# Performance work log

Hardware: AMD Instinct MI355X
Metric: run time of the kernel (lower is better)

Reference implementation:

```python
import jax, jax.numpy as jnp
import numpy as np
from jax import lax

B, T = 64, 512
VOCAB, EMBED, UNITS = 32000, 256, 512


def setup_inputs() -> dict:
    key = jax.random.key(0)
    ks = jax.random.split(key, 8)
    s = 0.05
    G = 4 * UNITS
    return {
        "encoder_input": jax.random.randint(ks[0], (B, T), 0, VOCAB, dtype=jnp.int32),
        "embedding": jax.random.normal(ks[1], (VOCAB, EMBED), jnp.float32) * s,
        "W_fwd": jax.random.normal(ks[2], (EMBED, G), jnp.float32) * s,
        "U_fwd": jax.random.normal(ks[3], (UNITS, G), jnp.float32) * s,
        "b_fwd": jnp.zeros((G,), jnp.float32),
        "W_bwd": jax.random.normal(ks[4], (EMBED, G), jnp.float32) * s,
        "U_bwd": jax.random.normal(ks[5], (UNITS, G), jnp.float32) * s,
        "b_bwd": jnp.zeros((G,), jnp.float32),
    }


def _lstm_scan(x, mask, W, Uw, b, reverse):
    """Masked LSTM over time. Keras semantics: at masked steps the (h, c)
    state is carried through unchanged and the emitted output repeats the
    previous hidden state (which for LSTM equals the carried h).
    x: [B, T, E] float, mask: [B, T] bool."""
    Bsz = x.shape[0]
    Uh = Uw.shape[0]
    # Precompute input projection for all timesteps: [B, T, 4U]
    xz = jnp.einsum("bte,eg->btg", x, W) + b

    def step(carry, inp):
        h, c = carry
        z_x, m = inp  # z_x: [B, 4U], m: [B]
        z = z_x + h @ Uw
        i, f, g, o = jnp.split(z, 4, axis=-1)  # Keras gate order i, f, c, o
        i = jax.nn.sigmoid(i)
        f = jax.nn.sigmoid(f)
        g = jnp.tanh(g)
        o = jax.nn.sigmoid(o)
        c_new = f * c + i * g
        h_new = o * jnp.tanh(c_new)
        m = m[:, None]
        h = jnp.where(m, h_new, h)
        c = jnp.where(m, c_new, c)
        return (h, c), h

    h0 = jnp.zeros((Bsz, Uh), x.dtype)
    c0 = jnp.zeros((Bsz, Uh), x.dtype)
    (h, c), ys = lax.scan(
        step, (h0, c0), (xz.swapaxes(0, 1), mask.T), reverse=reverse
    )
    # lax.scan with reverse=True stacks outputs in original time order,
    # matching Keras Bidirectional's reverse-then-re-reverse behavior.
    return ys.swapaxes(0, 1), h, c


def reference(encoder_input, embedding, W_fwd, U_fwd, b_fwd, W_bwd, U_bwd, b_bwd):
    mask = encoder_input != 0  # mask_zero=True
    emb = embedding[encoder_input]  # [B, T, E]
    out_f, h_f, c_f = _lstm_scan(emb, mask, W_fwd, U_fwd, b_fwd, reverse=False)
    out_b, h_b, c_b = _lstm_scan(emb, mask, W_bwd, U_bwd, b_bwd, reverse=True)
    encoder_output = jnp.concatenate([out_f, out_b], axis=-1)  # [B, T, 2U]
    final_state_h = jnp.concatenate([h_f, h_b], axis=-1)  # [B, 2U]
    final_state_c = jnp.concatenate([c_f, c_b], axis=-1)  # [B, 2U]
    # Dropout is identity at inference (training=False default).
    return encoder_output, final_state_h, final_state_c
```

## Files before the change

kernel.cpp:

```cpp
#include <hip/hip_runtime.h>
#include <cstdint>


#define B_ 64
#define T_ 512
#define E_ 256

typedef __attribute__((ext_vector_type(8))) short bf16x8;
typedef __attribute__((ext_vector_type(4))) float f32x4;
typedef __attribute__((ext_vector_type(2))) float f32x2;
typedef __attribute__((ext_vector_type(2))) unsigned u32x2;

__device__ __forceinline__ unsigned short f2bf(float x) {
  unsigned u = __float_as_uint(x);
  u += 0x7FFFu + ((u >> 16) & 1u);
  return (unsigned short)(u >> 16);
}
__device__ __forceinline__ float sigm(float x) { return 1.0f / (1.0f + __expf(-x)); }
__device__ __forceinline__ float tanh_(float x) { return 1.0f - 2.0f / (__expf(2.0f * x) + 1.0f); }

__global__ void prep_kernel(const int* __restrict__ enc, const float* __restrict__ emb,
                            unsigned short* __restrict__ o) {
  const int bi = blockIdx.x;
  const int t = bi >> 6, b = bi & 63;
  const int tok = enc[b * T_ + t];
  float4 v = ((const float4*)(emb + (size_t)tok * E_))[threadIdx.x];
  ushort4 w;
  w.x = f2bf(v.x); w.y = f2bf(v.y); w.z = f2bf(v.z); w.w = f2bf(v.w);
  ((ushort4*)(o + (size_t)t * (B_ * E_) + b * E_))[threadIdx.x] = w;
}

__global__ void prep_w(const float* __restrict__ Wf, const float* __restrict__ Uf,
                       const float* __restrict__ Wb, const float* __restrict__ Ub,
                       unsigned short* __restrict__ Uq, unsigned short* __restrict__ Wq) {
  int bi = blockIdx.x;
  const int ns = bi & 1; bi >>= 1;
  const int kk = bi % 24; bi /= 24;
  const int nh = bi & 1; bi >>= 1;
  const int cg = bi & 31; bi >>= 5;
  const int d = bi;
  const int lane = threadIdx.x;
  const int l15 = lane & 15, l4 = lane >> 4;
  const bool isU = (kk < 16);
  const float* src = isU ? (d ? Ub : Uf) : (d ? Wb : Wf);
  const int ks = isU ? kk : (kk - 16);
  const int col = (nh * 2 + ns) * 512 + cg * 16 + l15;
  const int row0 = ks * 32 + l4 * 8;
  bf16x8 f;
#pragma unroll
  for (int i = 0; i < 8; ++i) f[i] = (short)f2bf(src[(size_t)(row0 + i) * 2048 + col]);
  unsigned short* dst = isU
    ? Uq + ((size_t)(((d * 32 + cg) * 2 + nh) * 16 + ks) * 2 + ns) * 512 + lane * 8
    : Wq + ((size_t)(((d * 32 + cg) * 2 + nh) * 8 + ks) * 2 + ns) * 512 + lane * 8;
  *(bf16x8*)dst = f;
}

__global__ __launch_bounds__(256, 1)
void lstm_dag(const int* __restrict__ enc, const unsigned short* __restrict__ embq,
              const unsigned short* __restrict__ Uq, const unsigned short* __restrict__ Wq,
              const float* __restrict__ bfv, const float* __restrict__ bbv,
              unsigned short* __restrict__ Hst, f32x2* __restrict__ SC,
              int* __restrict__ flg, float* __restrict__ out) {
  const int s = blockIdx.x >> 6;
  const int inner = blockIdx.x & 63;
  const int d = inner >> 5;
  const int cg = inner & 31;
  const int tid = threadIdx.x;
  const int lane = tid & 63;
  const int wave = tid >> 6;
  const int mh = wave & 1, nh = wave >> 1;
  const int l15 = lane & 15, l4 = lane >> 4;
  const int u0 = cg * 16;
  const int t = d ? (T_ - 1 - s) : s;

  __shared__ float Z[64][68];

  const unsigned short* ub = Uq + ((size_t)((d * 32 + cg) * 2 + nh)) * (16 * 2 * 512);
  const unsigned short* wb = Wq + ((size_t)((d * 32 + cg) * 2 + nh)) * (8 * 2 * 512);
  bf16x8 u_frag[16][2];
#pragma unroll
  for (int ks = 0; ks < 16; ++ks)
#pragma unroll
    for (int ns = 0; ns < 2; ++ns)
      u_frag[ks][ns] = *(const bf16x8*)(ub + (size_t)(ks * 2 + ns) * 512 + lane * 8);
  bf16x8 w_frag[8][2];
#pragma unroll
  for (int ks = 0; ks < 8; ++ks)
#pragma unroll
    for (int ns = 0; ns < 2; ++ns)
      w_frag[ks][ns] = *(const bf16x8*)(wb + (size_t)(ks * 2 + ns) * 512 + lane * 8);

  bf16x8 apf[8][2];
  {
    const unsigned short* eT = embq + (size_t)t * (B_ * E_);
#pragma unroll
    for (int ks = 0; ks < 8; ++ks)
#pragma unroll
      for (int ms = 0; ms < 2; ++ms) {
        const int b = mh * 32 + ms * 16 + l15;
        apf[ks][ms] = *(const bf16x8*)(eT + b * E_ + ks * 32 + l4 * 8);
      }
  }
  const int eb = tid >> 2;
  const int uq = tid & 3;
  const int msk = enc[eb * T_ + t];
  const float* bd = d ? bbv : bfv;
  f32x4 bias[4];
#pragma unroll
  for (int g = 0; g < 4; ++g)
    bias[g] = *(const f32x4*)(bd + g * 512 + u0 + uq * 4);

  f32x4 acc[2][2];
#pragma unroll
  for (int ms = 0; ms < 2; ++ms)
#pragma unroll
    for (int ns = 0; ns < 2; ++ns) acc[ms][ns] = (f32x4)0.0f;

#pragma unroll
  for (int ks = 0; ks < 8; ++ks)
#pragma unroll
    for (int ms = 0; ms < 2; ++ms)
#pragma unroll
      for (int ns = 0; ns < 2; ++ns)
        acc[ms][ns] = __builtin_amdgcn_mfma_f32_16x16x32_bf16(apf[ks][ms], w_frag[ks][ns],
                                                              acc[ms][ns], 0, 0, 0);

  f32x4 hin0 = (f32x4)0.0f, hin1 = (f32x4)0.0f;

  if (s > 0) {
    if (wave == 0) {
      int* fp = flg + ((size_t)s * 2 + d) * 32;
      for (;;) {
        int v = __hip_atomic_load(fp + (lane & 31), __ATOMIC_RELAXED, __HIP_MEMORY_SCOPE_AGENT);
        if (__ballot(v == 0) == 0ull) break;
        __builtin_amdgcn_s_sleep(4);
      }
    }
    __syncthreads();
    __builtin_amdgcn_s_setprio(1);

    bf16x8 ha[16][2];
    {
      const char* Hrd = (const char*)(Hst + ((size_t)(s & 1) * 2 + d) * 32768);
      const char* lb = Hrd + (l4 >> 1) * 2048 + mh * 1024 + l15 * 32 + (l4 & 1) * 16;
      const char* b0p = lb + 0 * 8192 + 4096;
      const char* b1p = lb + 1 * 8192 + 4096;
      const char* b2p = lb + 2 * 8192 + 4096;
      const char* b3p = lb + 3 * 8192 + 4096;
      const char* b4p = lb + 4 * 8192 + 4096;
      const char* b5p = lb + 5 * 8192 + 4096;
      const char* b6p = lb + 6 * 8192 + 4096;
      const char* b7p = lb + 7 * 8192 + 4096;
      const char* sp0 = (const char*)(SC + ((size_t)(s & 1) * 2 + d) * 32768
                                      + (size_t)cg * 1024 + eb * 16 + uq * 4);
      asm volatile(
        "global_load_dwordx4 %0, %34, off offset:-4096 sc0 sc1\n\t"
        "global_load_dwordx4 %1, %34, off offset:-3584 sc0 sc1\n\t"
        "global_load_dwordx4 %2, %34, off offset:0 sc0 sc1\n\t"
        "global_load_dwordx4 %3, %34, off offset:512 sc0 sc1\n\t"
        "global_load_dwordx4 %4, %35, off offset:-4096 sc0 sc1\n\t"
        "global_load_dwordx4 %5, %35, off offset:-3584 sc0 sc1\n\t"
        "global_load_dwordx4 %6, %35, off offset:0 sc0 sc1\n\t"
        "global_load_dwordx4 %7, %35, off offset:512 sc0 sc1\n\t"
        "global_load_dwordx4 %8, %36, off offset:-4096 sc0 sc1\n\t"
        "global_load_dwordx4 %9, %36, off offset:-3584 sc0 sc1\n\t"
        "global_load_dwordx4 %10, %36, off offset:0 sc0 sc1\n\t"
        "global_load_dwordx4 %11, %36, off offset:512 sc0 sc1\n\t"
        "global_load_dwordx4 %12, %37, off offset:-4096 sc0 sc1\n\t"
        "global_load_dwordx4 %13, %37, off offset:-3584 sc0 sc1\n\t"
        "global_load_dwordx4 %14, %37, off offset:0 sc0 sc1\n\t"
        "global_load_dwordx4 %15, %37, off offset:512 sc0 sc1\n\t"
        "global_load_dwordx4 %16, %38, off offset:-4096 sc0 sc1\n\t"
        "global_load_dwordx4 %17, %38, off offset:-3584 sc0 sc1\n\t"
        "global_load_dwordx4 %18, %38, off offset:0 sc0 sc1\n\t"
        "global_load_dwordx4 %19, %38, off offset:512 sc0 sc1\n\t"
        "global_load_dwordx4 %20, %39, off offset:-4096 sc0 sc1\n\t"
        "global_load_dwordx4 %21, %39, off offset:-3584 sc0 sc1\n\t"
        "global_load_dwordx4 %22, %39, off offset:0 sc0 sc1\n\t"
        "global_load_dwordx4 %23, %39, off offset:512 sc0 sc1\n\t"
        "global_load_dwordx4 %24, %40, off offset:-4096 sc0 sc1\n\t"
        "global_load_dwordx4 %25, %40, off offset:-3584 sc0 sc1\n\t"
        "global_load_dwordx4 %26, %40, off offset:0 sc0 sc1\n\t"
        "global_load_dwordx4 %27, %40, off offset:512 sc0 sc1\n\t"
        "global_load_dwordx4 %28, %41, off offset:-4096 sc0 sc1\n\t"
        "global_load_dwordx4 %29, %41, off offset:-3584 sc0 sc1\n\t"
        "global_load_dwordx4 %30, %41, off offset:0 sc0 sc1\n\t"
        "global_load_dwordx4 %31, %41, off offset:512 sc0 sc1\n\t"
        "global_load_dwordx4 %32, %42, off sc0 sc1\n\t"
        "global_load_dwordx4 %33, %42, off offset:16 sc0 sc1\n\t"
        "s_waitcnt vmcnt(0)"
        : "=v"(ha[0][0]), "=v"(ha[0][1]), "=v"(ha[1][0]), "=v"(ha[1][1]),
          "=v"(ha[2][0]), "=v"(ha[2][1]), "=v"(ha[3][0]), "=v"(ha[3][1]),
          "=v"(ha[4][0]), "=v"(ha[4][1]), "=v"(ha[5][0]), "=v"(ha[5][1]),
          "=v"(ha[6][0]), "=v"(ha[6][1]), "=v"(ha[7][0]), "=v"(ha[7][1]),
          "=v"(ha[8][0]), "=v"(ha[8][1]), "=v"(ha[9][0]), "=v"(ha[9][1]),
          "=v"(ha[10][0]), "=v"(ha[10][1]), "=v"(ha[11][0]), "=v"(ha[11][1]),
          "=v"(ha[12][0]), "=v"(ha[12][1]), "=v"(ha[13][0]), "=v"(ha[13][1]),
          "=v"(ha[14][0]), "=v"(ha[14][1]), "=v"(ha[15][0]), "=v"(ha[15][1]),
          "=v"(hin0), "=v"(hin1)
        : "v"(b0p), "v"(b1p), "v"(b2p), "v"(b3p),
          "v"(b4p), "v"(b5p), "v"(b6p), "v"(b7p), "v"(sp0)
        : "memory");
    }
#pragma unroll
    for (int ks = 0; ks < 16; ++ks) {
      acc[0][0] = __builtin_amdgcn_mfma_f32_16x16x32_bf16(ha[ks][0], u_frag[ks][0], acc[0][0], 0, 0, 0);
      acc[0][1] = __builtin_amdgcn_mfma_f32_16x16x32_bf16(ha[ks][0], u_frag[ks][1], acc[0][1], 0, 0, 0);
      acc[1][0] = __builtin_amdgcn_mfma_f32_16x16x32_bf16(ha[ks][1], u_frag[ks][0], acc[1][0], 0, 0, 0);
      acc[1][1] = __builtin_amdgcn_mfma_f32_16x16x32_bf16(ha[ks][1], u_frag[ks][1], acc[1][1], 0, 0, 0);
    }
  }

#pragma unroll
  for (int ms = 0; ms < 2; ++ms)
#pragma unroll
    for (int ns = 0; ns < 2; ++ns)
#pragma unroll
      for (int r = 0; r < 4; ++r)
        Z[mh * 32 + ms * 16 + l4 * 4 + r][nh * 32 + ns * 16 + l15] = acc[ms][ns][r];
  __syncthreads();

  f32x4 vi = *(const f32x4*)&Z[eb][uq * 4];
  f32x4 vf = *(const f32x4*)&Z[eb][16 + uq * 4];
  f32x4 vg = *(const f32x4*)&Z[eb][32 + uq * 4];
  f32x4 vo = *(const f32x4*)&Z[eb][48 + uq * 4];
  float hv[4], cv[4];
  {
    const bool m = (msk != 0);
    float hi_[4] = {hin0[0], hin0[2], hin1[0], hin1[2]};
    float ci_[4] = {hin0[1], hin0[3], hin1[1], hin1[3]};
#pragma unroll
    for (int i = 0; i < 4; ++i) {
      float ig = sigm(vi[i] + bias[0][i]);
      float fg = sigm(vf[i] + bias[1][i]);
      float gg = tanh_(vg[i] + bias[2][i]);
      float og = sigm(vo[i] + bias[3][i]);
      float cn = fg * ci_[i] + ig * gg;
      float hn = og * tanh_(cn);
      hv[i] = m ? hn : hi_[i];
      cv[i] = m ? cn : ci_[i];
    }
  }

  {
    u32x2 hu;
    hu[0] = (unsigned)f2bf(hv[0]) | ((unsigned)f2bf(hv[1]) << 16);
    hu[1] = (unsigned)f2bf(hv[2]) | ((unsigned)f2bf(hv[3]) << 16);
    f32x4 sc0v, sc1v;
    sc0v[0] = hv[0]; sc0v[1] = cv[0]; sc0v[2] = hv[1]; sc0v[3] = cv[1];
    sc1v[0] = hv[2]; sc1v[1] = cv[2]; sc1v[2] = hv[3]; sc1v[3] = cv[3];
    char* hp = (char*)(Hst + ((size_t)((s + 1) & 1) * 2 + d) * 32768
                       + (size_t)cg * 1024 + eb * 16 + uq * 4);
    char* scp = (char*)(SC + ((size_t)((s + 1) & 1) * 2 + d) * 32768
                        + (size_t)cg * 1024 + eb * 16 + uq * 4);
    asm volatile(
      "global_store_dwordx2 %0, %2, off sc0 sc1\n\t"
      "global_store_dwordx4 %1, %3, off sc0 sc1\n\t"
      "global_store_dwordx4 %1, %4, off offset:16 sc0 sc1\n\t"
      "s_waitcnt vmcnt(0)"
      :: "v"(hp), "v"(scp), "v"(hu), "v"(sc0v), "v"(sc1v)
      : "memory");
  }
  __syncthreads();
  if (tid == 0)
    __hip_atomic_store(flg + ((size_t)(s + 1) * 2 + d) * 32 + cg, 1,
                       __ATOMIC_RELAXED, __HIP_MEMORY_SCOPE_AGENT);
  __builtin_amdgcn_s_setprio(0);

  {
    f32x4 ov, cvv;
#pragma unroll
    for (int i = 0; i < 4; ++i) { ov[i] = hv[i]; cvv[i] = cv[i]; }
    *(f32x4*)&out[((size_t)eb * T_ + t) * 1024 + d * 512 + u0 + uq * 4] = ov;
    if (s == T_ - 1) {
      *(f32x4*)&out[33554432u + (size_t)eb * 1024 + d * 512 + u0 + uq * 4] = ov;
      *(f32x4*)&out[33619968u + (size_t)eb * 1024 + d * 512 + u0 + uq * 4] = cvv;
    }
  }
}

__global__ __launch_bounds__(256, 1)
void lstm_step(const int s, const int* __restrict__ enc, const unsigned short* __restrict__ embq,
               const unsigned short* __restrict__ Uq, const unsigned short* __restrict__ Wq,
               const float* __restrict__ bfv, const float* __restrict__ bbv,
               unsigned short* __restrict__ Hbf, float* __restrict__ Hf32,
               float* __restrict__ Cst, float* __restrict__ out) {
  const int tid = threadIdx.x;
  const int lane = tid & 63;
  const int wave = tid >> 6;
  const int mh = wave & 1, nh = wave >> 1;
  const int l15 = lane & 15, l4 = lane >> 4;
  const int d = blockIdx.x >> 5;
  const int cg = blockIdx.x & 31;
  const int u0 = cg * 16;
  const int t = d ? (T_ - 1 - s) : s;

  __shared__ float Z[64][68];

  const unsigned short* ub = Uq + ((size_t)((d * 32 + cg) * 2 + nh)) * (16 * 2 * 512);
  const unsigned short* wb = Wq + ((size_t)((d * 32 + cg) * 2 + nh)) * (8 * 2 * 512);
  bf16x8 u_frag[16][2];
#pragma unroll
  for (int ks = 0; ks < 16; ++ks)
#pragma unroll
    for (int ns = 0; ns < 2; ++ns)
      u_frag[ks][ns] = *(const bf16x8*)(ub + (size_t)(ks * 2 + ns) * 512 + lane * 8);
  bf16x8 w_frag[8][2];
#pragma unroll
  for (int ks = 0; ks < 8; ++ks)
#pragma unroll
    for (int ns = 0; ns < 2; ++ns)
      w_frag[ks][ns] = *(const bf16x8*)(wb + (size_t)(ks * 2 + ns) * 512 + lane * 8);

  bf16x8 apf[8][2];
  {
    const unsigned short* eT = embq + (size_t)t * (B_ * E_);
#pragma unroll
    for (int ks = 0; ks < 8; ++ks)
#pragma unroll
      for (int ms = 0; ms < 2; ++ms) {
        const int b = mh * 32 + ms * 16 + l15;
        apf[ks][ms] = *(const bf16x8*)(eT + b * E_ + ks * 32 + l4 * 8);
      }
  }
  const int ej = tid & 15;
  const int ebg = tid >> 4;
  int mpf[4];
#pragma unroll
  for (int r = 0; r < 4; ++r) mpf[r] = enc[(ebg * 4 + r) * T_ + t];

  f32x4 acc[2][2];
#pragma unroll
  for (int ms = 0; ms < 2; ++ms)
#pragma unroll
    for (int ns = 0; ns < 2; ++ns) acc[ms][ns] = (f32x4)0.0f;

#pragma unroll
  for (int ks = 0; ks < 8; ++ks)
#pragma unroll
    for (int ms = 0; ms < 2; ++ms)
#pragma unroll
      for (int ns = 0; ns < 2; ++ns)
        acc[ms][ns] = __builtin_amdgcn_mfma_f32_16x16x32_bf16(apf[ks][ms], w_frag[ks][ns],
                                                              acc[ms][ns], 0, 0, 0);

  if (s > 0) {
    const unsigned short* Hrd = Hbf + ((size_t)((s & 1) * 2 + d)) * (B_ * 512);
    bf16x8 ha[16][2];
#pragma unroll
    for (int ks = 0; ks < 16; ++ks)
#pragma unroll
      for (int ms = 0; ms < 2; ++ms) {
        const int b = mh * 32 + ms * 16 + l15;
        ha[ks][ms] = *(const bf16x8*)(Hrd + (size_t)b * 512 + ks * 32 + l4 * 8);
      }
#pragma unroll
    for (int ks = 0; ks < 16; ++ks) {
      acc[0][0] = __builtin_amdgcn_mfma_f32_16x16x32_bf16(ha[ks][0], u_frag[ks][0], acc[0][0], 0, 0, 0);
      acc[0][1] = __builtin_amdgcn_mfma_f32_16x16x32_bf16(ha[ks][0], u_frag[ks][1], acc[0][1], 0, 0, 0);
      acc[1][0] = __builtin_amdgcn_mfma_f32_16x16x32_bf16(ha[ks][1], u_frag[ks][0], acc[1][0], 0, 0, 0);
      acc[1][1] = __builtin_amdgcn_mfma_f32_16x16x32_bf16(ha[ks][1], u_frag[ks][1], acc[1][1], 0, 0, 0);
    }
  }

#pragma unroll
  for (int ms = 0; ms < 2; ++ms)
#pragma unroll
    for (int ns = 0; ns < 2; ++ns)
#pragma unroll
      for (int r = 0; r < 4; ++r)
        Z[mh * 32 + ms * 16 + l4 * 4 + r][nh * 32 + ns * 16 + l15] = acc[ms][ns][r];
  __syncthreads();

  const float* bd = d ? bbv : bfv;
  float bias[4];
#pragma unroll
  for (int g = 0; g < 4; ++g) bias[g] = bd[g * 512 + u0 + ej];

  float* Hf = Hf32 + (size_t)d * (B_ * 512);
  float* Cf = Cst + (size_t)d * (B_ * 512);
  unsigned short* Hwr = Hbf + ((size_t)(((s + 1) & 1) * 2 + d)) * (B_ * 512);
  const bool last = (s == T_ - 1);
#pragma unroll
  for (int r = 0; r < 4; ++r) {
    const int b = ebg * 4 + r;
    const size_t si = (size_t)b * 512 + u0 + ej;
    float zi = Z[b][ej] + bias[0];
    float zf = Z[b][16 + ej] + bias[1];
    float zg = Z[b][32 + ej] + bias[2];
    float zo = Z[b][48 + ej] + bias[3];
    float ig = sigm(zi), fg = sigm(zf), gg = tanh_(zg), og = sigm(zo);
    float hp = Hf[si], cp = Cf[si];
    float cn = fg * cp + ig * gg;
    float hn = og * tanh_(cn);
    const bool m = (mpf[r] != 0);
    float hv = m ? hn : hp;
    float cv = m ? cn : cp;
    Hf[si] = hv;
    Cf[si] = cv;
    Hwr[si] = f2bf(hv);
    out[((size_t)b * T_ + t) * 1024 + d * 512 + u0 + ej] = hv;
    if (last) {
      out[33554432u + (size_t)b * 1024 + d * 512 + u0 + ej] = hv;
      out[33619968u + (size_t)b * 1024 + d * 512 + u0 + ej] = cv;
    }
  }
}

extern "C" void kernel_launch(void* const* d_in, const int* in_sizes, int n_in,
                              void* d_out, int out_size, void* d_ws, size_t ws_size,
                              hipStream_t stream) {
  const int* enc = (const int*)d_in[0];
  const float* emb = (const float*)d_in[1];
  const float* Wf = (const float*)d_in[2];
  const float* Uf = (const float*)d_in[3];
  const float* bf = (const float*)d_in[4];
  const float* Wb = (const float*)d_in[5];
  const float* Ub = (const float*)d_in[6];
  const float* bb = (const float*)d_in[7];
  float* out = (float*)d_out;
  char* ws = (char*)d_ws;

  unsigned short* embq = (unsigned short*)ws;
  unsigned short* Uq  = (unsigned short*)(ws + 16777216u);
  unsigned short* Wq  = (unsigned short*)(ws + 20971520u);

  const size_t OFF_HST = 23068672u;
  const size_t OFF_SC  = 23330816u;
  const size_t OFF_FLG = 25427968u;
  const size_t NEED    = 25559296u;

  prep_kernel<<<32768, 64, 0, stream>>>(enc, emb, embq);
  prep_w<<<6144, 64, 0, stream>>>(Wf, Uf, Wb, Ub, Uq, Wq);

  if (ws_size >= NEED) {
    unsigned short* Hst = (unsigned short*)(ws + OFF_HST);
    f32x2* SC = (f32x2*)(ws + OFF_SC);
    int*   flg = (int*)(ws + OFF_FLG);
    hipMemsetAsync(ws + OFF_SC, 0, NEED - OFF_SC, stream);
    lstm_dag<<<32768, 256, 0, stream>>>(enc, embq, Uq, Wq, bf, bb,
                                        Hst, SC, flg, out);
  } else {
    unsigned short* Hbf = (unsigned short*)(ws + 23068672u);
    float* Hf32 = (float*)(ws + 23330816u);
    float* Cst  = (float*)(ws + 23592960u);
    hipMemsetAsync(ws + 23068672u, 0, 786432u, stream);
    for (int s = 0; s < 512; ++s)
      lstm_step<<<64, 256, 0, stream>>>(s, enc, embq, Uq, Wq, bf, bb, Hbf, Hf32, Cst, out);
  }
}
```

Before: 3.155 ms.

## Stream hidden-state loads in chunks as producer flags become ready

Wave 0 polls the per-column-group flags and publishes through a shared-memory counter how many of the four 8-group chunks of the previous hidden state are complete; the block's own group is also required before chunk 0. The other waves spin on that counter and issue the global loads for each chunk as soon as it is ready, instead of waiting for all 32 producers behind a block barrier. This overlaps load latency with waiting on slower producers. It adds LDS spin loops across waves, and correctness depends on the relaxed flag reads being ordered before the sc0 sc1 data loads.

```diff
diff --git a/kernel.cpp b/kernel.cpp
--- a/kernel.cpp
+++ b/kernel.cpp
@@ -74,6 +74,7 @@
   const int t = d ? (T_ - 1 - s) : s;
 
   __shared__ float Z[64][68];
+  __shared__ int rdy;
 
   const unsigned short* ub = Uq + ((size_t)((d * 32 + cg) * 2 + nh)) * (16 * 2 * 512);
   const unsigned short* wb = Wq + ((size_t)((d * 32 + cg) * 2 + nh)) * (8 * 2 * 512);
@@ -128,79 +129,77 @@
   f32x4 hin0 = (f32x4)0.0f, hin1 = (f32x4)0.0f;
 
   if (s > 0) {
+    if (tid == 0) *(volatile int*)&rdy = 0;
+    __syncthreads();
+
     if (wave == 0) {
       int* fp = flg + ((size_t)s * 2 + d) * 32;
+      int got = 0;
       for (;;) {
         int v = __hip_atomic_load(fp + (lane & 31), __ATOMIC_RELAXED, __HIP_MEMORY_SCOPE_AGENT);
-        if (__ballot(v == 0) == 0ull) break;
-        __builtin_amdgcn_s_sleep(4);
-      }
-    }
-    __syncthreads();
-    __builtin_amdgcn_s_setprio(1);
+        unsigned long long ready = __ballot(v != 0);
+        int c = got;
+        while (c < 4) {
+          unsigned long long m = (0xFFull << (8 * c)) | (0xFFull << (32 + 8 * c));
+          if (c == 0) m |= (1ull << cg) | (1ull << (32 + cg));
+          if ((ready & m) == m) ++c; else break;
+        }
+        if (c > got) { got = c; if (lane == 0) *(volatile int*)&rdy = got; }
+        if (got == 4) break;
+      }
+    }
 
     bf16x8 ha[16][2];
     {
       const char* Hrd = (const char*)(Hst + ((size_t)(s & 1) * 2 + d) * 32768);
       const char* lb = Hrd + (l4 >> 1) * 2048 + mh * 1024 + l15 * 32 + (l4 & 1) * 16;
-      const char* b0p = lb + 0 * 8192 + 4096;
-      const char* b1p = lb + 1 * 8192 + 4096;
-      const char* b2p = lb + 2 * 8192 + 4096;
-      const char* b3p = lb + 3 * 8192 + 4096;
-      const char* b4p = lb + 4 * 8192 + 4096;
-      const char* b5p = lb + 5 * 8192 + 4096;
-      const char* b6p = lb + 6 * 8192 + 4096;
-      const char* b7p = lb + 7 * 8192 + 4096;
       const char* sp0 = (const char*)(SC + ((size_t)(s & 1) * 2 + d) * 32768
                                       + (size_t)cg * 1024 + eb * 16 + uq * 4);
-      asm volatile(
-        "global_load_dwordx4 %0, %34, off offset:-4096 sc0 sc1\n\t"
-        "global_load_dwordx4 %1, %34, off offset:-3584 sc0 sc1\n\t"
-        "global_load_dwordx4 %2, %34, off offset:0 sc0 sc1\n\t"
-        "global_load_dwordx4 %3, %34, off offset:512 sc0 sc1\n\t"
-        "global_load_dwordx4 %4, %35, off offset:-4096 sc0 sc1\n\t"
-        "global_load_dwordx4 %5, %35, off offset:-3584 sc0 sc1\n\t"
-        "global_load_dwordx4 %6, %35, off offset:0 sc0 sc1\n\t"
-        "global_load_dwordx4 %7, %35, off offset:512 sc0 sc1\n\t"
-        "global_load_dwordx4 %8, %36, off offset:-4096 sc0 sc1\n\t"
-        "global_load_dwordx4 %9, %36, off offset:-3584 sc0 sc1\n\t"
-        "global_load_dwordx4 %10, %36, off offset:0 sc0 sc1\n\t"
-        "global_load_dwordx4 %11, %36, off offset:512 sc0 sc1\n\t"
-        "global_load_dwordx4 %12, %37, off offset:-4096 sc0 sc1\n\t"
-        "global_load_dwordx4 %13, %37, off offset:-3584 sc0 sc1\n\t"
-        "global_load_dwordx4 %14, %37, off offset:0 sc0 sc1\n\t"
-        "global_load_dwordx4 %15, %37, off offset:512 sc0 sc1\n\t"
-        "global_load_dwordx4 %16, %38, off offset:-4096 sc0 sc1\n\t"
-        "global_load_dwordx4 %17, %38, off offset:-3584 sc0 sc1\n\t"
-        "global_load_dwordx4 %18, %38, off offset:0 sc0 sc1\n\t"
-        "global_load_dwordx4 %19, %38, off offset:512 sc0 sc1\n\t"
-        "global_load_dwordx4 %20, %39, off offset:-4096 sc0 sc1\n\t"
-        "global_load_dwordx4 %21, %39, off offset:-3584 sc0 sc1\n\t"
-        "global_load_dwordx4 %22, %39, off offset:0 sc0 sc1\n\t"
-        "global_load_dwordx4 %23, %39, off offset:512 sc0 sc1\n\t"
-        "global_load_dwordx4 %24, %40, off offset:-4096 sc0 sc1\n\t"
-        "global_load_dwordx4 %25, %40, off offset:-3584 sc0 sc1\n\t"
-        "global_load_dwordx4 %26, %40, off offset:0 sc0 sc1\n\t"
-        "global_load_dwordx4 %27, %40, off offset:512 sc0 sc1\n\t"
-        "global_load_dwordx4 %28, %41, off offset:-4096 sc0 sc1\n\t"
-        "global_load_dwordx4 %29, %41, off offset:-3584 sc0 sc1\n\t"
-        "global_load_dwordx4 %30, %41, off offset:0 sc0 sc1\n\t"
-        "global_load_dwordx4 %31, %41, off offset:512 sc0 sc1\n\t"
-        "global_load_dwordx4 %32, %42, off sc0 sc1\n\t"
-        "global_load_dwordx4 %33, %42, off offset:16 sc0 sc1\n\t"
-        "s_waitcnt vmcnt(0)"
-        : "=v"(ha[0][0]), "=v"(ha[0][1]), "=v"(ha[1][0]), "=v"(ha[1][1]),
-          "=v"(ha[2][0]), "=v"(ha[2][1]), "=v"(ha[3][0]), "=v"(ha[3][1]),
-          "=v"(ha[4][0]), "=v"(ha[4][1]), "=v"(ha[5][0]), "=v"(ha[5][1]),
-          "=v"(ha[6][0]), "=v"(ha[6][1]), "=v"(ha[7][0]), "=v"(ha[7][1]),
-          "=v"(ha[8][0]), "=v"(ha[8][1]), "=v"(ha[9][0]), "=v"(ha[9][1]),
-          "=v"(ha[10][0]), "=v"(ha[10][1]), "=v"(ha[11][0]), "=v"(ha[11][1]),
-          "=v"(ha[12][0]), "=v"(ha[12][1]), "=v"(ha[13][0]), "=v"(ha[13][1]),
-          "=v"(ha[14][0]), "=v"(ha[14][1]), "=v"(ha[15][0]), "=v"(ha[15][1]),
-          "=v"(hin0), "=v"(hin1)
-        : "v"(b0p), "v"(b1p), "v"(b2p), "v"(b3p),
-          "v"(b4p), "v"(b5p), "v"(b6p), "v"(b7p), "v"(sp0)
-        : "memory");
+      while (*(volatile int*)&rdy < 1) {}
+      __builtin_amdgcn_s_setprio(1);
+      {
+        const char* pA = lb + 4096;
+        const char* pB = lb + 8192 + 4096;
+        asm volatile(
+          "global_load_dwordx4 %0, %10, off offset:-4096 sc0 sc1\n\t"
+          "global_load_dwordx4 %1, %10, off offset:-3584 sc0 sc1\n\t"
+          "global_load_dwordx4 %2, %10, off offset:0 sc0 sc1\n\t"
+          "global_load_dwordx4 %3, %10, off offset:512 sc0 sc1\n\t"
+          "global_load_dwordx4 %4, %11, off offset:-4096 sc0 sc1\n\t"
+          "global_load_dwordx4 %5, %11, off offset:-3584 sc0 sc1\n\t"
+          "global_load_dwordx4 %6, %11, off offset:0 sc0 sc1\n\t"
+          "global_load_dwordx4 %7, %11, off offset:512 sc0 sc1\n\t"
+          "global_load_dwordx4 %8, %12, off sc0 sc1\n\t"
+          "global_load_dwordx4 %9, %12, off offset:16 sc0 sc1"
+          : "=v"(ha[0][0]), "=v"(ha[0][1]), "=v"(ha[1][0]), "=v"(ha[1][1]),
+            "=v"(ha[2][0]), "=v"(ha[2][1]), "=v"(ha[3][0]), "=v"(ha[3][1]),
+            "=v"(hin0), "=v"(hin1)
+          : "v"(pA), "v"(pB), "v"(sp0)
+          : "memory");
+      }
+#pragma unroll
+      for (int c = 1; c < 4; ++c) {
+        while (*(volatile int*)&rdy < c + 1) {}
+        const char* pA = lb + (size_t)(2 * c) * 8192 + 4096;
+        const char* pB = lb + (size_t)(2 * c + 1) * 8192 + 4096;
+        asm volatile(
+          "global_load_dwordx4 %0, %8, off offset:-4096 sc0 sc1\n\t"
+          "global_load_dwordx4 %1, %8, off offset:-3584 sc0 sc1\n\t"
+          "global_load_dwordx4 %2, %8, off offset:0 sc0 sc1\n\t"
+          "global_load_dwordx4 %3, %8, off offset:512 sc0 sc1\n\t"
+          "global_load_dwordx4 %4, %9, off offset:-4096 sc0 sc1\n\t"
+          "global_load_dwordx4 %5, %9, off offset:-3584 sc0 sc1\n\t"
+          "global_load_dwordx4 %6, %9, off offset:0 sc0 sc1\n\t"
+          "global_load_dwordx4 %7, %9, off offset:512 sc0 sc1"
+          : "=v"(ha[4 * c][0]), "=v"(ha[4 * c][1]),
+            "=v"(ha[4 * c + 1][0]), "=v"(ha[4 * c + 1][1]),
+            "=v"(ha[4 * c + 2][0]), "=v"(ha[4 * c + 2][1]),
+            "=v"(ha[4 * c + 3][0]), "=v"(ha[4 * c + 3][1])
+          : "v"(pA), "v"(pB)
+          : "memory");
+      }
+      asm volatile("s_waitcnt vmcnt(0)" ::: "memory");
+      __builtin_amdgcn_sched_barrier(0);
     }
 #pragma unroll
     for (int ks = 0; ks < 16; ++ks) {
```

Measured after the change: 3.402 ms. 1.08x slower.
